# Performance work log

Measured on AMD Instinct MI355X. Metric: run time of the kernel, lower is better.

Reference implementation:

```python
import jax, jax.numpy as jnp
import numpy as np

EMBED_DIM = 1024
NUM_HEADS = 16
HEAD_DIM = EMBED_DIM // NUM_HEADS
SCALE = float(np.sqrt(HEAD_DIM))


def setup_inputs() -> dict:
    key = jax.random.key(0)
    ks = jax.random.split(key, 7)
    B, S, E = 2, 2048, EMBED_DIM
    query = jax.random.normal(ks[0], (B, S, E), dtype=jnp.float32)
    key_t = jax.random.normal(ks[1], (B, S, E), dtype=jnp.float32)
    value = jax.random.normal(ks[2], (B, S, E), dtype=jnp.float32)
    # nn.Linear(E, E, bias=False): weight shape (out, in); y = x @ W.T
    std = 1.0 / np.sqrt(E)
    Wq = jax.random.uniform(ks[3], (E, E), jnp.float32, -std, std)
    Wk = jax.random.uniform(ks[4], (E, E), jnp.float32, -std, std)
    Wv = jax.random.uniform(ks[5], (E, E), jnp.float32, -std, std)
    Wo = jax.random.uniform(ks[6], (E, E), jnp.float32, -std, std)
    return {"query": query, "key": key_t, "value": value,
            "Wq": Wq, "Wk": Wk, "Wv": Wv, "Wo": Wo}


def reference(query, key, value, Wq, Wk, Wv, Wo):
    B, S, E = query.shape
    H, D = NUM_HEADS, HEAD_DIM
    q = (query @ Wq.T).reshape(B, S, H, D).transpose(0, 2, 1, 3)  # [B,H,S,D]
    k = (key @ Wk.T).reshape(B, S, H, D).transpose(0, 2, 1, 3)
    v = (value @ Wv.T).reshape(B, S, H, D).transpose(0, 2, 1, 3)
    scores = jnp.einsum('bhqd,bhkd->bhqk', q, k) / SCALE  # [B,H,S,S]
    attn = jax.nn.softmax(scores, axis=-1)
    out = jnp.einsum('bhqk,bhkd->bhqd', attn, v)  # [B,H,S,D]
    out = out.transpose(0, 2, 1, 3).reshape(B, S, E)
    return out @ Wo.T
```

## Files before the change

### kernel.cpp

```cpp
#include <hip/hip_runtime.h>
#include <hip/hip_bf16.h>
#include <math.h>

typedef float f32x4 __attribute__((ext_vector_type(4)));
typedef __bf16 bf16x8 __attribute__((ext_vector_type(8)));
typedef unsigned short u16;
typedef u16 u16x8 __attribute__((ext_vector_type(8)));
typedef u16 u16x4 __attribute__((ext_vector_type(4)));

__device__ __forceinline__ u16 f2bf(float f) {
    unsigned u = __builtin_bit_cast(unsigned, f);
    u = (u + 0x7fffu + ((u >> 16) & 1u)) >> 16;
    return (u16)u;
}
__device__ __forceinline__ unsigned pack2_rhu(float a, float b) {
    return __builtin_amdgcn_perm(__builtin_bit_cast(unsigned, b) + 0x8000u,
                                 __builtin_bit_cast(unsigned, a) + 0x8000u,
                                 0x07060302u);
}

#if __has_builtin(__builtin_amdgcn_exp2f)
#define EXP2(x) __builtin_amdgcn_exp2f(x)
#else
#define EXP2(x) exp2f(x)
#endif

__device__ __forceinline__ void gload16(const u16* g, u16* l) {
    __builtin_amdgcn_global_load_lds(
        (const __attribute__((address_space(1))) unsigned int*)(g),
        (__attribute__((address_space(3))) unsigned int*)(l), 16, 0, 0);
}

__global__ __launch_bounds__(256) void cast_all(
    const float* __restrict__ q, const float* __restrict__ k, const float* __restrict__ v,
    const float* __restrict__ wq, const float* __restrict__ wk, const float* __restrict__ wv,
    const float* __restrict__ wo, u16* __restrict__ dst) {
    int i = blockIdx.x * 256 + threadIdx.x;
    const float* src;
    int off;
    if (i < 3145728) {
        int seg = i >> 20;
        src = (seg == 0) ? q : (seg == 1) ? k : v;
        off = i - (seg << 20);
    } else {
        int j = (i - 3145728) >> 18;
        src = (j == 0) ? wq : (j == 1) ? wk : (j == 2) ? wv : wo;
        off = (i - 3145728) - (j << 18);
    }
    float4 val = ((const float4*)src)[off];
    u16x4 o4;
    o4.x = f2bf(val.x); o4.y = f2bf(val.y); o4.z = f2bf(val.z); o4.w = f2bf(val.w);
    ((u16x4*)dst)[i] = o4;
}

__global__ __launch_bounds__(256) void qkv_gemm(
    const u16* __restrict__ Xq, const u16* __restrict__ Xk, const u16* __restrict__ Xv,
    const u16* __restrict__ Wq, const u16* __restrict__ Wk, const u16* __restrict__ Wv,
    u16* __restrict__ Qo, u16* __restrict__ Ko, u16* __restrict__ Vto) {
    constexpr int K = 1024;
    const int blk = blockIdx.x;
    const int xb = blk / 96;
    const int zb = (blk % 96) >> 5;
    const int yb = blk & 31;
    const int z = zb;
    const u16* __restrict__ A = (z == 0) ? Xq : (z == 1) ? Xk : Xv;
    const u16* __restrict__ W = (z == 0) ? Wq : (z == 1) ? Wk : Wv;
    u16* __restrict__ Out = (z == 0) ? Qo : (z == 1) ? Ko : Vto;

    __shared__ __align__(16) u16 As[128 * 64];
    __shared__ __align__(16) u16 Bs[128 * 64];

    const int t = threadIdx.x;
    const int lane = t & 63, wave = t >> 6;
    const int quad = lane >> 4, c = lane & 15, cx = c & 7;
    const int wr = (wave >> 1) * 64, wc = (wave & 1) * 64;
    const int rowA0 = yb * 128;
    const int colB0 = xb * 128;

    const int l3 = lane >> 3, l7 = lane & 7;
    const int chs = (l7 ^ l3) << 3;
    const u16* gA[4];
    const u16* gB[4];
    u16* lA[4];
    u16* lB[4];
#pragma unroll
    for (int i = 0; i < 4; ++i) {
        int row = wave * 32 + i * 8 + l3;
        gA[i] = A + (size_t)(rowA0 + row) * K + chs;
        gB[i] = W + (size_t)(colB0 + row) * K + chs;
        lA[i] = As + (wave * 256 + i * 64) * 8;
        lB[i] = Bs + (wave * 256 + i * 64) * 8;
    }

    const f32x4 zero4 = {0.f, 0.f, 0.f, 0.f};
    f32x4 acc[4][4];
#pragma unroll
    for (int i = 0; i < 4; ++i)
#pragma unroll
        for (int j = 0; j < 4; ++j) acc[i][j] = zero4;

    for (int kt = 0; kt < K; kt += 64) {
        __syncthreads();
#pragma unroll
        for (int i = 0; i < 4; ++i) {
            gload16(gA[i] + kt, lA[i]);
            gload16(gB[i] + kt, lB[i]);
        }
        __syncthreads();
#pragma unroll
        for (int ks = 0; ks < 2; ++ks) {
            const int co = ((ks * 4 + quad) ^ cx) << 3;
            bf16x8 af[4], bfr[4];
#pragma unroll
            for (int i = 0; i < 4; ++i)
                af[i] = *(const bf16x8*)(As + (wr + i * 16 + c) * 64 + co);
#pragma unroll
            for (int j = 0; j < 4; ++j)
                bfr[j] = *(const bf16x8*)(Bs + (wc + j * 16 + c) * 64 + co);
            if (z == 2) {
#pragma unroll
                for (int i = 0; i < 4; ++i)
#pragma unroll
                    for (int j = 0; j < 4; ++j)
                        acc[i][j] = __builtin_amdgcn_mfma_f32_16x16x32_bf16(bfr[j], af[i], acc[i][j], 0, 0, 0);
            } else {
#pragma unroll
                for (int i = 0; i < 4; ++i)
#pragma unroll
                    for (int j = 0; j < 4; ++j)
                        acc[i][j] = __builtin_amdgcn_mfma_f32_16x16x32_bf16(af[i], bfr[j], acc[i][j], 0, 0, 0);
            }
        }
    }

    const float scale = (z == 0) ? 0.18033688011112042f : 1.0f;
#pragma unroll
    for (int i = 0; i < 4; ++i) {
#pragma unroll
        for (int j = 0; j < 4; ++j) {
#pragma unroll
            for (int r = 0; r < 4; ++r) {
                float v = acc[i][j][r];
                if (z == 2) {
                    int n = colB0 + wc + j * 16 + quad * 4 + r;
                    int m = rowA0 + wr + i * 16 + c;
                    int b = m >> 11, s = m & 2047, h = n >> 6, d = n & 63;
                    Out[((((b << 4) | h) << 6) + d) * 2048 + s] = f2bf(v);
                } else {
                    int m = rowA0 + wr + i * 16 + quad * 4 + r;
                    int n = colB0 + wc + j * 16 + c;
                    int b = m >> 11, s = m & 2047, h = n >> 6, d = n & 63;
                    Out[((((b << 4) | h) * 2048 + s) << 6) + d] = f2bf(v * scale);
                }
            }
        }
    }
}

__global__ __launch_bounds__(256, 2) void out_gemm(const u16* __restrict__ A,
                                                   const u16* __restrict__ W,
                                                   float* __restrict__ Out) {
    constexpr int K = 1024;
    __shared__ __align__(16) u16 As[64 * 64];
    __shared__ __align__(16) u16 Bs[128 * 64];
    const int blk = blockIdx.x;
    const int yb = blk & 63;
    const int xb = blk >> 6;
    const int t = threadIdx.x;
    const int lane = t & 63, wave = t >> 6;
    const int quad = lane >> 4, c = lane & 15, cx = c & 7;
    const int wr = (wave >> 1) * 32, wc = (wave & 1) * 64;
    const int rowA0 = yb * 64;
    const int colB0 = xb * 128;

    const int l3 = lane >> 3, l7 = lane & 7;
    const int chs = (l7 ^ l3) << 3;
    const u16* gA[2];
    const u16* gB[4];
    u16* lA[2];
    u16* lB[4];
#pragma unroll
    for (int i = 0; i < 2; ++i) {
        int row = wave * 16 + i * 8 + l3;
        gA[i] = A + (size_t)(rowA0 + row) * K + chs;
        lA[i] = As + (wave * 128 + i * 64) * 8;
    }
#pragma unroll
    for (int i = 0; i < 4; ++i) {
        int row = wave * 32 + i * 8 + l3;
        gB[i] = W + (size_t)(colB0 + row) * K + chs;
        lB[i] = Bs + (wave * 256 + i * 64) * 8;
    }

    const f32x4 zero4 = {0.f, 0.f, 0.f, 0.f};
    f32x4 acc[2][4];
#pragma unroll
    for (int i = 0; i < 2; ++i)
#pragma unroll
        for (int j = 0; j < 4; ++j) acc[i][j] = zero4;

    for (int kt = 0; kt < K; kt += 64) {
        __syncthreads();
#pragma unroll
        for (int i = 0; i < 2; ++i) gload16(gA[i] + kt, lA[i]);
#pragma unroll
        for (int i = 0; i < 4; ++i) gload16(gB[i] + kt, lB[i]);
        __syncthreads();
#pragma unroll
        for (int ks = 0; ks < 2; ++ks) {
            const int co = ((ks * 4 + quad) ^ cx) << 3;
            bf16x8 af[2], bfr[4];
#pragma unroll
            for (int i = 0; i < 2; ++i)
                af[i] = *(const bf16x8*)(As + (wr + i * 16 + c) * 64 + co);
#pragma unroll
            for (int j = 0; j < 4; ++j)
                bfr[j] = *(const bf16x8*)(Bs + (wc + j * 16 + c) * 64 + co);
#pragma unroll
            for (int i = 0; i < 2; ++i)
#pragma unroll
                for (int j = 0; j < 4; ++j)
                    acc[i][j] = __builtin_amdgcn_mfma_f32_16x16x32_bf16(af[i], bfr[j], acc[i][j], 0, 0, 0);
        }
    }
#pragma unroll
    for (int i = 0; i < 2; ++i)
#pragma unroll
        for (int j = 0; j < 4; ++j)
#pragma unroll
            for (int r = 0; r < 4; ++r) {
                int m = rowA0 + wr + i * 16 + quad * 4 + r;
                int n = colB0 + wc + j * 16 + c;
                Out[(m << 10) + n] = acc[i][j][r];
            }
}

__global__ __launch_bounds__(256, 2) void flash_attn(const u16* __restrict__ Qp,
                                                     const u16* __restrict__ Kp,
                                                     const u16* __restrict__ Vt,
                                                     u16* __restrict__ Ob) {
    constexpr int S = 2048;
    const int blk = blockIdx.x;
    const int j = blk & 31;
    const int bh = ((j & 7) << 2) | (j >> 3);
    const int b = bh >> 4, h = bh & 15;
    const int t = threadIdx.x, wave = t >> 6, lane = t & 63;
    const int quad = lane >> 4, c = lane & 15, cx = c & 7;
    const int qw = (blk >> 5) * 128 + wave * 32;
    const u16* Qb = Qp + (bh * S + qw) * 64;
    const u16* Kb = Kp + (bh * S) * 64;
    const u16* Vb = Vt + bh * 64 * S;

    __shared__ __align__(16) u16 Ks[2][64 * 64];
    __shared__ __align__(16) u16 Vs[2][64 * 64];
    __shared__ __align__(16) u16 Ps[4][32 * 64];
    u16* Pw = &Ps[wave][0];

    bf16x8 qf[2][2];
#pragma unroll
    for (int qt = 0; qt < 2; ++qt)
#pragma unroll
        for (int hf = 0; hf < 2; ++hf)
            qf[qt][hf] = *(const bf16x8*)(Qb + (qt * 16 + c) * 64 + hf * 32 + quad * 8);

    u16x8 ou;
#pragma unroll
    for (int i = 0; i < 8; ++i) ou[i] = 0x3F80;
    const bf16x8 onesf = __builtin_bit_cast(bf16x8, ou);

    const int l3 = lane >> 3, l7 = lane & 7;
    const int chs = (l7 ^ l3) << 3;
    const u16* gK[2];
    const u16* gV[2];
    int lbase[2];
#pragma unroll
    for (int i = 0; i < 2; ++i) {
        int row = wave * 16 + i * 8 + l3;
        gK[i] = Kb + row * 64 + chs;
        gV[i] = Vb + row * 2048 + chs;
        lbase[i] = (wave * 128 + i * 64) * 8;
    }
#pragma unroll
    for (int i = 0; i < 2; ++i) {
        gload16(gK[i], &Ks[0][lbase[i]]);
        gload16(gV[i], &Vs[0][lbase[i]]);
    }
    __syncthreads();

    const f32x4 zero4 = {0.f, 0.f, 0.f, 0.f};
    f32x4 o[2][4];
    f32x4 ol[2];
#pragma unroll
    for (int qt = 0; qt < 2; ++qt) {
        ol[qt] = zero4;
#pragma unroll
        for (int t2 = 0; t2 < 4; ++t2) o[qt][t2] = zero4;
    }

    const int co0 = (quad ^ cx) << 3, co1 = ((4 + quad) ^ cx) << 3;

    for (int it = 0; it < S / 64; ++it) {
        const int cur = it & 1;
        if (it + 1 < S / 64) {
#pragma unroll
            for (int i = 0; i < 2; ++i) {
                gload16(gK[i] + (it + 1) * 4096, &Ks[cur ^ 1][lbase[i]]);
                gload16(gV[i] + (it + 1) * 64, &Vs[cur ^ 1][lbase[i]]);
            }
        }
        const u16* Kc = &Ks[cur][0];
        const u16* Vc = &Vs[cur][0];
        f32x4 sc[4][2];
#pragma unroll
        for (int kt = 0; kt < 4; ++kt) {
            const int krow = (kt * 16 + c) * 64;
            bf16x8 kf0 = *(const bf16x8*)(Kc + krow + co0);
            bf16x8 kf1 = *(const bf16x8*)(Kc + krow + co1);
#pragma unroll
            for (int qt = 0; qt < 2; ++qt) {
                f32x4 zz = zero4;
                zz = __builtin_amdgcn_mfma_f32_16x16x32_bf16(kf0, qf[qt][0], zz, 0, 0, 0);
                zz = __builtin_amdgcn_mfma_f32_16x16x32_bf16(kf1, qf[qt][1], zz, 0, 0, 0);
                sc[kt][qt] = zz;
            }
        }
#pragma unroll
        for (int kt = 0; kt < 4; ++kt) {
            const int pchunk = ((kt * 2 + (quad >> 1)) ^ cx) << 3;
#pragma unroll
            for (int qt = 0; qt < 2; ++qt) {
                float p0 = EXP2(sc[kt][qt][0]);
                float p1 = EXP2(sc[kt][qt][1]);
                float p2 = EXP2(sc[kt][qt][2]);
                float p3 = EXP2(sc[kt][qt][3]);
                uint2 pk;
                pk.x = pack2_rhu(p0, p1);
                pk.y = pack2_rhu(p2, p3);
                *(uint2*)(Pw + (qt * 16 + c) * 64 + pchunk + (quad & 1) * 4) = pk;
            }
        }
        __asm__ __volatile__("s_waitcnt lgkmcnt(0)" ::: "memory");
        bf16x8 pf[2][2];
#pragma unroll
        for (int qt = 0; qt < 2; ++qt) {
            pf[qt][0] = *(const bf16x8*)(Pw + (qt * 16 + c) * 64 + co0);
            pf[qt][1] = *(const bf16x8*)(Pw + (qt * 16 + c) * 64 + co1);
        }
#pragma unroll
        for (int qt = 0; qt < 2; ++qt) {
            ol[qt] = __builtin_amdgcn_mfma_f32_16x16x32_bf16(pf[qt][0], onesf, ol[qt], 0, 0, 0);
            ol[qt] = __builtin_amdgcn_mfma_f32_16x16x32_bf16(pf[qt][1], onesf, ol[qt], 0, 0, 0);
        }
#pragma unroll
        for (int t2 = 0; t2 < 4; ++t2) {
            const int vrow = (t2 * 16 + c) * 64;
            bf16x8 vf0 = *(const bf16x8*)(Vc + vrow + co0);
            bf16x8 vf1 = *(const bf16x8*)(Vc + vrow + co1);
#pragma unroll
            for (int qt = 0; qt < 2; ++qt) {
                o[qt][t2] = __builtin_amdgcn_mfma_f32_16x16x32_bf16(pf[qt][0], vf0, o[qt][t2], 0, 0, 0);
                o[qt][t2] = __builtin_amdgcn_mfma_f32_16x16x32_bf16(pf[qt][1], vf1, o[qt][t2], 0, 0, 0);
            }
        }
        __syncthreads();
    }
#pragma unroll
    for (int qt = 0; qt < 2; ++qt)
#pragma unroll
        for (int r = 0; r < 4; ++r) {
            float inv = 1.f / ol[qt][r];
            int row = qw + qt * 16 + quad * 4 + r;
            int base = ((b * S + row) * 16 + h) * 64;
#pragma unroll
            for (int t2 = 0; t2 < 4; ++t2)
                Ob[base + t2 * 16 + c] = f2bf(o[qt][t2][r] * inv);
        }
}

extern "C" void kernel_launch(void* const* d_in, const int* in_sizes, int n_in,
                              void* d_out, int out_size, void* d_ws, size_t ws_size,
                              hipStream_t stream) {
    const float* q  = (const float*)d_in[0];
    const float* k  = (const float*)d_in[1];
    const float* v  = (const float*)d_in[2];
    const float* wq = (const float*)d_in[3];
    const float* wk = (const float*)d_in[4];
    const float* wv = (const float*)d_in[5];
    const float* wo = (const float*)d_in[6];

    u16* ws = (u16*)d_ws;
    u16* qb  = ws;
    u16* kb  = ws + 4194304;
    u16* vb  = ws + 8388608;
    u16* wqb = ws + 12582912;
    u16* wkb = ws + 13631488;
    u16* wvb = ws + 14680064;
    u16* wob = ws + 15728640;
    u16* Qp  = ws + 16777216;
    u16* Kp  = ws + 20971520;
    u16* Vtp = ws + 25165824;
    u16* Obf = ws + 29360128;

    cast_all<<<16384, 256, 0, stream>>>(q, k, v, wq, wk, wv, wo, ws);

    qkv_gemm<<<768, 256, 0, stream>>>(qb, kb, vb, wqb, wkb, wvb, Qp, Kp, Vtp);

    flash_attn<<<512, 256, 0, stream>>>(Qp, Kp, Vtp, Obf);

    out_gemm<<<512, 256, 0, stream>>>(Obf, wob, (float*)d_out);
}
```

Before: 214.2 us.

## Double-buffer GEMM LDS tiles and widen flash-attention blocks to 8 waves

Both projection GEMMs now use two LDS buffers. The next K-tile is fetched while the current one is consumed, which drops one barrier per iteration and hides global load latency. The flash attention kernel moves from 4 to 8 waves per block, covering 256 query rows, so each K/V tile in LDS is shared by twice as many waves and each wave issues one load per tile instead of two. The costs are doubled LDS use in the GEMMs, fewer resident blocks, the out_gemm occupancy hint being dropped, and half as many attention blocks to spread over the CUs.

After: 216.5 us. No clear change (+1.1%).

```diff
diff --git a/kernel.cpp b/kernel.cpp
--- a/kernel.cpp
+++ b/kernel.cpp
@@ -58,6 +58,7 @@
     const u16* __restrict__ Wq, const u16* __restrict__ Wk, const u16* __restrict__ Wv,
     u16* __restrict__ Qo, u16* __restrict__ Ko, u16* __restrict__ Vto) {
     constexpr int K = 1024;
+    constexpr int BUF = 128 * 64;
     const int blk = blockIdx.x;
     const int xb = blk / 96;
     const int zb = (blk % 96) >> 5;
@@ -67,8 +68,8 @@
     const u16* __restrict__ W = (z == 0) ? Wq : (z == 1) ? Wk : Wv;
     u16* __restrict__ Out = (z == 0) ? Qo : (z == 1) ? Ko : Vto;
 
-    __shared__ __align__(16) u16 As[128 * 64];
-    __shared__ __align__(16) u16 Bs[128 * 64];
+    __shared__ __align__(16) u16 As[2 * BUF];
+    __shared__ __align__(16) u16 Bs[2 * BUF];
 
     const int t = threadIdx.x;
     const int lane = t & 63, wave = t >> 6;
@@ -99,24 +100,34 @@
 #pragma unroll
         for (int j = 0; j < 4; ++j) acc[i][j] = zero4;
 
-    for (int kt = 0; kt < K; kt += 64) {
+#pragma unroll
+    for (int i = 0; i < 4; ++i) {
+        gload16(gA[i], lA[i]);
+        gload16(gB[i], lB[i]);
+    }
+
+    for (int it = 0; it < 16; ++it) {
         __syncthreads();
-#pragma unroll
-        for (int i = 0; i < 4; ++i) {
-            gload16(gA[i] + kt, lA[i]);
-            gload16(gB[i] + kt, lB[i]);
-        }
-        __syncthreads();
+        if (it + 1 < 16) {
+            const int nb = ((it + 1) & 1) * BUF;
+            const int kt = (it + 1) * 64;
+#pragma unroll
+            for (int i = 0; i < 4; ++i) {
+                gload16(gA[i] + kt, lA[i] + nb);
+                gload16(gB[i] + kt, lB[i] + nb);
+            }
+        }
+        const int so = (it & 1) * BUF;
 #pragma unroll
         for (int ks = 0; ks < 2; ++ks) {
             const int co = ((ks * 4 + quad) ^ cx) << 3;
             bf16x8 af[4], bfr[4];
 #pragma unroll
             for (int i = 0; i < 4; ++i)
-                af[i] = *(const bf16x8*)(As + (wr + i * 16 + c) * 64 + co);
+                af[i] = *(const bf16x8*)(As + so + (wr + i * 16 + c) * 64 + co);
 #pragma unroll
             for (int j = 0; j < 4; ++j)
-                bfr[j] = *(const bf16x8*)(Bs + (wc + j * 16 + c) * 64 + co);
+                bfr[j] = *(const bf16x8*)(Bs + so + (wc + j * 16 + c) * 64 + co);
             if (z == 2) {
 #pragma unroll
                 for (int i = 0; i < 4; ++i)
@@ -157,12 +168,14 @@
     }
 }
 
-__global__ __launch_bounds__(256, 2) void out_gemm(const u16* __restrict__ A,
-                                                   const u16* __restrict__ W,
-                                                   float* __restrict__ Out) {
+__global__ __launch_bounds__(256) void out_gemm(const u16* __restrict__ A,
+                                                const u16* __restrict__ W,
+                                                float* __restrict__ Out) {
     constexpr int K = 1024;
-    __shared__ __align__(16) u16 As[64 * 64];
-    __shared__ __align__(16) u16 Bs[128 * 64];
+    constexpr int ABUF = 64 * 64;
+    constexpr int BBUF = 128 * 64;
+    __shared__ __align__(16) u16 As[2 * ABUF];
+    __shared__ __align__(16) u16 Bs[2 * BBUF];
     const int blk = blockIdx.x;
     const int yb = blk & 63;
     const int xb = blk >> 6;
@@ -199,23 +212,33 @@
 #pragma unroll
         for (int j = 0; j < 4; ++j) acc[i][j] = zero4;
 
-    for (int kt = 0; kt < K; kt += 64) {
+#pragma unroll
+    for (int i = 0; i < 2; ++i) gload16(gA[i], lA[i]);
+#pragma unroll
+    for (int i = 0; i < 4; ++i) gload16(gB[i], lB[i]);
+
+    for (int it = 0; it < 16; ++it) {
         __syncthreads();
-#pragma unroll
-        for (int i = 0; i < 2; ++i) gload16(gA[i] + kt, lA[i]);
-#pragma unroll
-        for (int i = 0; i < 4; ++i) gload16(gB[i] + kt, lB[i]);
-        __syncthreads();
+        if (it + 1 < 16) {
+            const int kt = (it + 1) * 64;
+            const int nsel = (it + 1) & 1;
+#pragma unroll
+            for (int i = 0; i < 2; ++i) gload16(gA[i] + kt, lA[i] + nsel * ABUF);
+#pragma unroll
+            for (int i = 0; i < 4; ++i) gload16(gB[i] + kt, lB[i] + nsel * BBUF);
+        }
+        const int soA = (it & 1) * ABUF;
+        const int soB = (it & 1) * BBUF;
 #pragma unroll
         for (int ks = 0; ks < 2; ++ks) {
             const int co = ((ks * 4 + quad) ^ cx) << 3;
             bf16x8 af[2], bfr[4];
 #pragma unroll
             for (int i = 0; i < 2; ++i)
-                af[i] = *(const bf16x8*)(As + (wr + i * 16 + c) * 64 + co);
+                af[i] = *(const bf16x8*)(As + soA + (wr + i * 16 + c) * 64 + co);
 #pragma unroll
             for (int j = 0; j < 4; ++j)
-                bfr[j] = *(const bf16x8*)(Bs + (wc + j * 16 + c) * 64 + co);
+                bfr[j] = *(const bf16x8*)(Bs + soB + (wc + j * 16 + c) * 64 + co);
 #pragma unroll
             for (int i = 0; i < 2; ++i)
 #pragma unroll
@@ -235,25 +258,24 @@
             }
 }
 
-__global__ __launch_bounds__(256, 2) void flash_attn(const u16* __restrict__ Qp,
-                                                     const u16* __restrict__ Kp,
-                                                     const u16* __restrict__ Vt,
-                                                     u16* __restrict__ Ob) {
+__global__ __launch_bounds__(512) void flash_attn(const u16* __restrict__ Qp,
+                                                  const u16* __restrict__ Kp,
+                                                  const u16* __restrict__ Vt,
+                                                  u16* __restrict__ Ob) {
     constexpr int S = 2048;
     const int blk = blockIdx.x;
-    const int j = blk & 31;
-    const int bh = ((j & 7) << 2) | (j >> 3);
+    const int bh = ((blk & 7) << 2) | ((blk >> 3) & 3);
     const int b = bh >> 4, h = bh & 15;
     const int t = threadIdx.x, wave = t >> 6, lane = t & 63;
     const int quad = lane >> 4, c = lane & 15, cx = c & 7;
-    const int qw = (blk >> 5) * 128 + wave * 32;
+    const int qw = (blk >> 5) * 256 + wave * 32;
     const u16* Qb = Qp + (bh * S + qw) * 64;
     const u16* Kb = Kp + (bh * S) * 64;
     const u16* Vb = Vt + bh * 64 * S;
 
     __shared__ __align__(16) u16 Ks[2][64 * 64];
     __shared__ __align__(16) u16 Vs[2][64 * 64];
-    __shared__ __align__(16) u16 Ps[4][32 * 64];
+    __shared__ __align__(16) u16 Ps[8][32 * 64];
     u16* Pw = &Ps[wave][0];
 
     bf16x8 qf[2][2];
@@ -270,21 +292,13 @@
 
     const int l3 = lane >> 3, l7 = lane & 7;
     const int chs = (l7 ^ l3) << 3;
-    const u16* gK[2];
-    const u16* gV[2];
-    int lbase[2];
-#pragma unroll
-    for (int i = 0; i < 2; ++i) {
-        int row = wave * 16 + i * 8 + l3;
-        gK[i] = Kb + row * 64 + chs;
-        gV[i] = Vb + row * 2048 + chs;
-        lbase[i] = (wave * 128 + i * 64) * 8;
-    }
-#pragma unroll
-    for (int i = 0; i < 2; ++i) {
-        gload16(gK[i], &Ks[0][lbase[i]]);
-        gload16(gV[i], &Vs[0][lbase[i]]);
-    }
+    const int row = wave * 8 + l3;
+    const u16* gK = Kb + row * 64 + chs;
+    const u16* gV = Vb + row * 2048 + chs;
+    const int lbase = wave * 512;
+
+    gload16(gK, &Ks[0][lbase]);
+    gload16(gV, &Vs[0][lbase]);
     __syncthreads();
 
     const f32x4 zero4 = {0.f, 0.f, 0.f, 0.f};
@@ -302,11 +316,8 @@
     for (int it = 0; it < S / 64; ++it) {
         const int cur = it & 1;
         if (it + 1 < S / 64) {
-#pragma unroll
-            for (int i = 0; i < 2; ++i) {
-                gload16(gK[i] + (it + 1) * 4096, &Ks[cur ^ 1][lbase[i]]);
-                gload16(gV[i] + (it + 1) * 64, &Vs[cur ^ 1][lbase[i]]);
-            }
+            gload16(gK + (it + 1) * 4096, &Ks[cur ^ 1][lbase]);
+            gload16(gV + (it + 1) * 64, &Vs[cur ^ 1][lbase]);
         }
         const u16* Kc = &Ks[cur][0];
         const u16* Vc = &Vs[cur][0];
@@ -369,8 +380,8 @@
 #pragma unroll
         for (int r = 0; r < 4; ++r) {
             float inv = 1.f / ol[qt][r];
-            int row = qw + qt * 16 + quad * 4 + r;
-            int base = ((b * S + row) * 16 + h) * 64;
+            int rw = qw + qt * 16 + quad * 4 + r;
+            int base = ((b * S + rw) * 16 + h) * 64;
 #pragma unroll
             for (int t2 = 0; t2 < 4; ++t2)
                 Ob[base + t2 * 16 + c] = f2bf(o[qt][t2][r] * inv);
@@ -405,7 +416,7 @@
 
     qkv_gemm<<<768, 256, 0, stream>>>(qb, kb, vb, wqb, wkb, wvb, Qp, Kp, Vtp);
 
-    flash_attn<<<512, 256, 0, stream>>>(Qp, Kp, Vtp, Obf);
+    flash_attn<<<256, 512, 0, stream>>>(Qp, Kp, Vtp, Obf);
 
     out_gemm<<<512, 256, 0, stream>>>(Obf, wob, (float*)d_out);
 }
```
